# Performance work log

Measured on AMD Instinct MI355X. Metric: run time of the kernel, lower is better.

## Reference

```python
import jax, jax.numpy as jnp
import numpy as np

# Transformer config constants (from init_kwargs)
SRF = 3.0                 # spatial_receptive_field
SRF2 = SRF * SRF
ALPHA = 2.0
BETA = 8.0
GAMMA = 16.0
RES = jnp.array([0.5, 0.5, 0.5], dtype=jnp.float32)   # relative_positional_gresolution
N_BUCKETS = 2 * 8 + 1                                  # 2*beta + 1 = 17
MUL = jnp.array([N_BUCKETS ** 2, N_BUCKETS, 1], dtype=jnp.float32)  # [289,17,1]
SLICES_PER_ROT = 2


def setup_inputs() -> dict:
    key = jax.random.key(0)
    k1, k2 = jax.random.split(key)
    N = 3072
    # LiDAR-like point coordinates in a 10m cube; receptive field 3.0 makes radius filter selective
    xyz = jax.random.uniform(k1, (N, 3), dtype=jnp.float32) * 10.0
    # grid columns: [batch, block, gx, gy, gz]; values < 128 per the torch assert
    grid = jax.random.randint(k2, (N, 5), 0, 8, dtype=jnp.int32)
    return {"xyz": xyz, "grid": grid}


def _bucket_base(x):
    # from_dxyz_to_bucket_base, res.size(0)==3 branch
    x = x / RES
    x_abs = jnp.abs(x)
    log_ratio = jnp.log(jnp.maximum(x_abs, 1e-6) / ALPHA) / np.log(GAMMA / ALPHA)
    sup = jnp.minimum(jnp.round(ALPHA - (BETA - ALPHA) * log_ratio), BETA)
    sup = jnp.sign(x) * sup
    return BETA + jnp.where(x_abs <= ALPHA, jnp.round(x), sup)


def reference(xyz, grid):
    # no-kvp path of jit_compute_interactions, expressed as dense [N,N] pair masks
    batch = grid[:, 0]
    block = grid[:, 1]
    coords = grid[:, 2:]            # grid_look[:, 1:]

    # batch equality filter (meshgrid + batch==batch)
    batch_eq = batch[:, None] == batch[None, :]
    # causal block filter: block[iq] <= block[ik]
    block_le = block[:, None] <= block[None, :]

    # force_keep_neighbours: adjacent voxels within the same block
    coord_adj = jnp.max(jnp.abs(coords[:, None, :] - coords[None, :, :]), axis=-1) <= 1
    forcekeep = coord_adj & (block[:, None] == block[None, :])

    # coarse spatial hash on xy: ceil(xy / srf), neighbor cells only
    xy_coarse = jnp.ceil(xyz[:, :2] / SRF).astype(jnp.int32)
    keep_coarse = jnp.max(jnp.abs(xy_coarse[:, None, :] - xy_coarse[None, :, :]), axis=-1) <= 1

    # pairwise deltas (torch uses fp16 here; fp32 kept for numerical clarity) [N,N,3]
    dxyz = xyz[:, None, :] - xyz[None, :, :]
    keepr = jnp.sum(dxyz * dxyz, axis=-1) <= SRF2

    mask = batch_eq & block_le & (forcekeep | keep_coarse) & (forcekeep | keepr)

    dxyz_m = jnp.where(mask[..., None], dxyz, 0.0)

    # from_dxyz_to_bucket_mul: log-bucketize each axis, flatten via mul_buckets
    buckets = jnp.sum(MUL * _bucket_base(dxyz_m), axis=-1).astype(jnp.int32)
    buckets = jnp.where(mask, buckets, 0)

    # dscanid = scanid[ik] - scanid[iq], scanid = block // slices_per_rotation
    scanid = block // SLICES_PER_ROT
    dscanid = jnp.where(mask, scanid[None, :] - scanid[:, None], 0)

    return dxyz_m, buckets, dscanid, mask
```

## Files before the change

### kernel.cpp

```cpp
#include <hip/hip_runtime.h>
#include <cmath>


__device__ __forceinline__ float bucket_base(float v) {
    const float x  = v * 2.0f;
    const float xa = fabsf(x);
    if (xa <= 2.0f) {
        return 8.0f + rintf(x);
    }
    const float lr = logf(fmaxf(xa, 1e-6f) * 0.5f) / 2.0794415416798357f;
    const float sup = fminf(rintf(2.0f - 6.0f * lr), 8.0f);
    return 8.0f + ((x > 0.0f) ? sup : -sup);
}

__global__ __launch_bounds__(256) void pair_kernel(
    const float* __restrict__ xyz, const int* __restrict__ grid,
    float* __restrict__ out, int N) {
#pragma clang fp contract(off)
    const int jq = blockIdx.x * blockDim.x + threadIdx.x;
    const int j0 = jq << 2;
    const int i  = blockIdx.y;
    if (j0 >= N) return;

    const float xi = xyz[3 * i + 0];
    const float yi = xyz[3 * i + 1];
    const float zi = xyz[3 * i + 2];
    const int bat_i = grid[5 * i + 0];
    const int blk_i = grid[5 * i + 1];
    const int c0i = grid[5 * i + 2];
    const int c1i = grid[5 * i + 3];
    const int c2i = grid[5 * i + 4];
    const int xci = (int)ceilf(xi / 3.0f);
    const int yci = (int)ceilf(yi / 3.0f);
    const int scan_i = blk_i >> 1;

    const float4* pv = reinterpret_cast<const float4*>(xyz + (size_t)3 * j0);
    const float4 p0 = pv[0], p1 = pv[1], p2 = pv[2];
    const int4* gv = reinterpret_cast<const int4*>(grid + (size_t)5 * j0);
    const int4 g0 = gv[0], g1 = gv[1], g2 = gv[2], g3 = gv[3], g4 = gv[4];

    const float jx[4]  = {p0.x, p0.w, p1.z, p2.y};
    const float jy[4]  = {p0.y, p1.x, p1.w, p2.z};
    const float jz[4]  = {p0.z, p1.y, p2.x, p2.w};
    const int   jbat[4] = {g0.x, g1.y, g2.z, g3.w};
    const int   jblk[4] = {g0.y, g1.z, g2.w, g4.x};
    const int   jc0[4]  = {g0.z, g1.w, g3.x, g4.y};
    const int   jc1[4]  = {g0.w, g2.x, g3.y, g4.z};
    const int   jc2[4]  = {g1.x, g2.y, g3.z, g4.w};

    float dxm[4], dym[4], dzm[4];
    bool  mk[4];
    bool  any = false;
#pragma unroll
    for (int k = 0; k < 4; ++k) {
        const float dx = xi - jx[k];
        const float dy = yi - jy[k];
        const float dz = zi - jz[k];
        const bool batch_eq = (bat_i == jbat[k]);
        const bool block_le = (blk_i <= jblk[k]);
        const int  cadj = max(max(abs(c0i - jc0[k]), abs(c1i - jc1[k])),
                              abs(c2i - jc2[k]));
        const bool forcekeep = (cadj <= 1) && (blk_i == jblk[k]);
        const int xcj = (int)ceilf(jx[k] / 3.0f);
        const int ycj = (int)ceilf(jy[k] / 3.0f);
        const bool keep_coarse = max(abs(xci - xcj), abs(yci - ycj)) <= 1;
        const float d2 = dx * dx + dy * dy + dz * dz;
        const bool keepr = (d2 <= 9.0f);
        const bool m = batch_eq && block_le &&
                       (forcekeep || keep_coarse) && (forcekeep || keepr);
        mk[k] = m;
        any |= m;
        dxm[k] = m ? dx : 0.0f;
        dym[k] = m ? dy : 0.0f;
        dzm[k] = m ? dz : 0.0f;
    }

    const size_t NN   = (size_t)N * (size_t)N;
    const size_t base = (size_t)i * (size_t)N + (size_t)j0;
    float4* o_dxyz = reinterpret_cast<float4*>(out + 3 * base);
    float4* o_bkt  = reinterpret_cast<float4*>(out + NN * 3 + base);
    float4* o_dsc  = reinterpret_cast<float4*>(out + NN * 4 + base);
    float4* o_msk  = reinterpret_cast<float4*>(out + NN * 5 + base);

    if (__ballot(any ? 1 : 0) == 0ULL) {
        const float4 z = make_float4(0.0f, 0.0f, 0.0f, 0.0f);
        o_dxyz[0] = z; o_dxyz[1] = z; o_dxyz[2] = z;
        o_bkt[0]  = z; o_dsc[0]  = z; o_msk[0]  = z;
        return;
    }

    float bf[4], df[4], mf[4];
#pragma unroll
    for (int k = 0; k < 4; ++k) {
        if (mk[k]) {
            const float b0 = bucket_base(dxm[k]);
            const float b1 = bucket_base(dym[k]);
            const float b2 = bucket_base(dzm[k]);
            const float bsum = (289.0f * b0 + 17.0f * b1) + b2;
            bf[k] = (float)(int)bsum;
            df[k] = (float)((jblk[k] >> 1) - scan_i);
            mf[k] = 1.0f;
        } else {
            bf[k] = 0.0f; df[k] = 0.0f; mf[k] = 0.0f;
        }
    }

    o_dxyz[0] = make_float4(dxm[0], dym[0], dzm[0], dxm[1]);
    o_dxyz[1] = make_float4(dym[1], dzm[1], dxm[2], dym[2]);
    o_dxyz[2] = make_float4(dzm[2], dxm[3], dym[3], dzm[3]);
    o_bkt[0]  = make_float4(bf[0], bf[1], bf[2], bf[3]);
    o_dsc[0]  = make_float4(df[0], df[1], df[2], df[3]);
    o_msk[0]  = make_float4(mf[0], mf[1], mf[2], mf[3]);
}

extern "C" void kernel_launch(void* const* d_in, const int* in_sizes, int n_in,
                              void* d_out, int out_size, void* d_ws, size_t ws_size,
                              hipStream_t stream) {
    const float* xyz  = (const float*)d_in[0];
    const int*   grid = (const int*)d_in[1];
    float*       out  = (float*)d_out;
    const int N = in_sizes[0] / 3;

    const int BLOCK = 256;
    const int jquads = N / 4;
    dim3 gdim((jquads + BLOCK - 1) / BLOCK, N, 1);
    pair_kernel<<<gdim, dim3(BLOCK, 1, 1), 0, stream>>>(xyz, grid, out, N);
}
```

Measured before the change: 219.6 us.

## Map each thread to one contiguous output float4 across all six output planes

The kernel is restructured so each thread writes one float4 of the flat output buffer, in order, instead of each thread writing scattered float4s into six separate planes. The aim is fully contiguous, coalesced streaming writes. In exchange, the mask is recomputed for every plane (dxyz, buckets, dscanid, mask), which adds redundant loads and ALU work. The dxyz plane also evaluates pairs individually, with a divide by N and a modulo by 3. A template specialisation for N=3072 lets the compiler turn those divides into constant arithmetic.

```diff
diff --git a/kernel.cpp b/kernel.cpp
--- a/kernel.cpp
+++ b/kernel.cpp
@@ -13,26 +13,47 @@
     return 8.0f + ((x > 0.0f) ? sup : -sup);
 }
 
-__global__ __launch_bounds__(256) void pair_kernel(
+template<int CN>
+__device__ __forceinline__ void one_pair(
     const float* __restrict__ xyz, const int* __restrict__ grid,
-    float* __restrict__ out, int N) {
+    int Nrt, int p, float& dxm, float& dym, float& dzm)
+{
 #pragma clang fp contract(off)
-    const int jq = blockIdx.x * blockDim.x + threadIdx.x;
-    const int j0 = jq << 2;
-    const int i  = blockIdx.y;
-    if (j0 >= N) return;
+    const int N = CN ? CN : Nrt;
+    const int i = (int)((unsigned)p / (unsigned)N);
+    const int j = p - i * N;
+    const float xi = xyz[3*i+0], yi = xyz[3*i+1], zi = xyz[3*i+2];
+    const float xj = xyz[3*j+0], yj = xyz[3*j+1], zj = xyz[3*j+2];
+    const int bat_i = grid[5*i+0], blk_i = grid[5*i+1];
+    const int c0i = grid[5*i+2], c1i = grid[5*i+3], c2i = grid[5*i+4];
+    const int bat_j = grid[5*j+0], blk_j = grid[5*j+1];
+    const int c0j = grid[5*j+2], c1j = grid[5*j+3], c2j = grid[5*j+4];
+    const float dx = xi - xj, dy = yi - yj, dz = zi - zj;
+    const bool batch_eq = (bat_i == bat_j);
+    const bool block_le = (blk_i <= blk_j);
+    const int  cadj = max(max(abs(c0i-c0j), abs(c1i-c1j)), abs(c2i-c2j));
+    const bool forcekeep = (cadj <= 1) && (blk_i == blk_j);
+    const int xci = (int)ceilf(xi/3.0f), yci = (int)ceilf(yi/3.0f);
+    const int xcj = (int)ceilf(xj/3.0f), ycj = (int)ceilf(yj/3.0f);
+    const bool keep_coarse = max(abs(xci-xcj), abs(yci-ycj)) <= 1;
+    const float d2 = dx*dx + dy*dy + dz*dz;
+    const bool keepr = (d2 <= 9.0f);
+    const bool m = batch_eq && block_le &&
+                   (forcekeep || keep_coarse) && (forcekeep || keepr);
+    dxm = m ? dx : 0.0f; dym = m ? dy : 0.0f; dzm = m ? dz : 0.0f;
+}
 
-    const float xi = xyz[3 * i + 0];
-    const float yi = xyz[3 * i + 1];
-    const float zi = xyz[3 * i + 2];
-    const int bat_i = grid[5 * i + 0];
-    const int blk_i = grid[5 * i + 1];
-    const int c0i = grid[5 * i + 2];
-    const int c1i = grid[5 * i + 3];
-    const int c2i = grid[5 * i + 4];
-    const int xci = (int)ceilf(xi / 3.0f);
-    const int yci = (int)ceilf(yi / 3.0f);
-    const int scan_i = blk_i >> 1;
+__device__ __forceinline__ void quad_mask(
+    const float* __restrict__ xyz, const int* __restrict__ grid,
+    int i, int j0,
+    float dxm[4], float dym[4], float dzm[4], bool mk[4],
+    int jblk[4], int& blk_i, bool& any)
+{
+#pragma clang fp contract(off)
+    const float xi = xyz[3*i+0], yi = xyz[3*i+1], zi = xyz[3*i+2];
+    const int bat_i = grid[5*i+0]; blk_i = grid[5*i+1];
+    const int c0i = grid[5*i+2], c1i = grid[5*i+3], c2i = grid[5*i+4];
+    const int xci = (int)ceilf(xi/3.0f), yci = (int)ceilf(yi/3.0f);
 
     const float4* pv = reinterpret_cast<const float4*>(xyz + (size_t)3 * j0);
     const float4 p0 = pv[0], p1 = pv[1], p2 = pv[2];
@@ -43,24 +64,22 @@
     const float jy[4]  = {p0.y, p1.x, p1.w, p2.z};
     const float jz[4]  = {p0.z, p1.y, p2.x, p2.w};
     const int   jbat[4] = {g0.x, g1.y, g2.z, g3.w};
-    const int   jblk[4] = {g0.y, g1.z, g2.w, g4.x};
+    const int   jb[4]   = {g0.y, g1.z, g2.w, g4.x};
     const int   jc0[4]  = {g0.z, g1.w, g3.x, g4.y};
     const int   jc1[4]  = {g0.w, g2.x, g3.y, g4.z};
     const int   jc2[4]  = {g1.x, g2.y, g3.z, g4.w};
 
-    float dxm[4], dym[4], dzm[4];
-    bool  mk[4];
-    bool  any = false;
+    any = false;
 #pragma unroll
     for (int k = 0; k < 4; ++k) {
         const float dx = xi - jx[k];
         const float dy = yi - jy[k];
         const float dz = zi - jz[k];
         const bool batch_eq = (bat_i == jbat[k]);
-        const bool block_le = (blk_i <= jblk[k]);
+        const bool block_le = (blk_i <= jb[k]);
         const int  cadj = max(max(abs(c0i - jc0[k]), abs(c1i - jc1[k])),
                               abs(c2i - jc2[k]));
-        const bool forcekeep = (cadj <= 1) && (blk_i == jblk[k]);
+        const bool forcekeep = (cadj <= 1) && (blk_i == jb[k]);
         const int xcj = (int)ceilf(jx[k] / 3.0f);
         const int ycj = (int)ceilf(jy[k] / 3.0f);
         const bool keep_coarse = max(abs(xci - xcj), abs(yci - ycj)) <= 1;
@@ -68,49 +87,90 @@
         const bool keepr = (d2 <= 9.0f);
         const bool m = batch_eq && block_le &&
                        (forcekeep || keep_coarse) && (forcekeep || keepr);
-        mk[k] = m;
-        any |= m;
+        mk[k] = m; any |= m;
+        jblk[k] = jb[k];
         dxm[k] = m ? dx : 0.0f;
         dym[k] = m ? dy : 0.0f;
         dzm[k] = m ? dz : 0.0f;
     }
+}
 
-    const size_t NN   = (size_t)N * (size_t)N;
-    const size_t base = (size_t)i * (size_t)N + (size_t)j0;
-    float4* o_dxyz = reinterpret_cast<float4*>(out + 3 * base);
-    float4* o_bkt  = reinterpret_cast<float4*>(out + NN * 3 + base);
-    float4* o_dsc  = reinterpret_cast<float4*>(out + NN * 4 + base);
-    float4* o_msk  = reinterpret_cast<float4*>(out + NN * 5 + base);
+template<int CN>
+__global__ __launch_bounds__(256) void linear_kernel(
+    const float* __restrict__ xyz, const int* __restrict__ grid,
+    float* __restrict__ out, int Nrt)
+{
+    const int N = CN ? CN : Nrt;
+    const unsigned NN = (unsigned)N * (unsigned)N;
+    const unsigned t = blockIdx.x * blockDim.x + threadIdx.x;
+    const unsigned e = t * 4u;
+    if (e >= 6u * NN) return;
+    float4* dst = reinterpret_cast<float4*>(out + (size_t)e);
 
-    if (__ballot(any ? 1 : 0) == 0ULL) {
-        const float4 z = make_float4(0.0f, 0.0f, 0.0f, 0.0f);
-        o_dxyz[0] = z; o_dxyz[1] = z; o_dxyz[2] = z;
-        o_bkt[0]  = z; o_dsc[0]  = z; o_msk[0]  = z;
+    if (e < 3u * NN) {
+        const unsigned c0 = e % 3u;
+        const int p0 = (int)(e / 3u);
+        float a0, a1, a2, b0, b1, b2;
+        one_pair<CN>(xyz, grid, N, p0,     a0, a1, a2);
+        one_pair<CN>(xyz, grid, N, p0 + 1, b0, b1, b2);
+        float4 v;
+        if (c0 == 0u)      v = make_float4(a0, a1, a2, b0);
+        else if (c0 == 1u) v = make_float4(a1, a2, b0, b1);
+        else               v = make_float4(a2, b0, b1, b2);
+        *dst = v;
         return;
     }
 
-    float bf[4], df[4], mf[4];
+    float dx[4], dy[4], dz[4];
+    bool  mk[4];
+    int   jblk[4], blk_i;
+    bool  any;
+
+    if (e < 4u * NN) {
+        const int p = (int)(e - 3u * NN);
+        const int i = (int)((unsigned)p / (unsigned)N);
+        const int j0 = p - i * N;
+        quad_mask(xyz, grid, i, j0, dx, dy, dz, mk, jblk, blk_i, any);
+        if (__ballot(any ? 1 : 0) == 0ULL) {
+            *dst = make_float4(0.0f, 0.0f, 0.0f, 0.0f);
+            return;
+        }
+        float bf[4];
 #pragma unroll
-    for (int k = 0; k < 4; ++k) {
-        if (mk[k]) {
-            const float b0 = bucket_base(dxm[k]);
-            const float b1 = bucket_base(dym[k]);
-            const float b2 = bucket_base(dzm[k]);
-            const float bsum = (289.0f * b0 + 17.0f * b1) + b2;
-            bf[k] = (float)(int)bsum;
-            df[k] = (float)((jblk[k] >> 1) - scan_i);
-            mf[k] = 1.0f;
-        } else {
-            bf[k] = 0.0f; df[k] = 0.0f; mf[k] = 0.0f;
+        for (int k = 0; k < 4; ++k) {
+            if (mk[k]) {
+                const float q0 = bucket_base(dx[k]);
+                const float q1 = bucket_base(dy[k]);
+                const float q2 = bucket_base(dz[k]);
+                const float bsum = (289.0f * q0 + 17.0f * q1) + q2;
+                bf[k] = (float)(int)bsum;
+            } else {
+                bf[k] = 0.0f;
+            }
         }
+        *dst = make_float4(bf[0], bf[1], bf[2], bf[3]);
+    } else if (e < 5u * NN) {
+        const int p = (int)(e - 4u * NN);
+        const int i = (int)((unsigned)p / (unsigned)N);
+        const int j0 = p - i * N;
+        quad_mask(xyz, grid, i, j0, dx, dy, dz, mk, jblk, blk_i, any);
+        const int scan_i = blk_i >> 1;
+        float df[4];
+#pragma unroll
+        for (int k = 0; k < 4; ++k)
+            df[k] = mk[k] ? (float)((jblk[k] >> 1) - scan_i) : 0.0f;
+        *dst = make_float4(df[0], df[1], df[2], df[3]);
+    } else {
+        const int p = (int)(e - 5u * NN);
+        const int i = (int)((unsigned)p / (unsigned)N);
+        const int j0 = p - i * N;
+        quad_mask(xyz, grid, i, j0, dx, dy, dz, mk, jblk, blk_i, any);
+        float mf[4];
+#pragma unroll
+        for (int k = 0; k < 4; ++k)
+            mf[k] = mk[k] ? 1.0f : 0.0f;
+        *dst = make_float4(mf[0], mf[1], mf[2], mf[3]);
     }
-
-    o_dxyz[0] = make_float4(dxm[0], dym[0], dzm[0], dxm[1]);
-    o_dxyz[1] = make_float4(dym[1], dzm[1], dxm[2], dym[2]);
-    o_dxyz[2] = make_float4(dzm[2], dxm[3], dym[3], dzm[3]);
-    o_bkt[0]  = make_float4(bf[0], bf[1], bf[2], bf[3]);
-    o_dsc[0]  = make_float4(df[0], df[1], df[2], df[3]);
-    o_msk[0]  = make_float4(mf[0], mf[1], mf[2], mf[3]);
 }
 
 extern "C" void kernel_launch(void* const* d_in, const int* in_sizes, int n_in,
@@ -121,8 +181,13 @@
     float*       out  = (float*)d_out;
     const int N = in_sizes[0] / 3;
 
+    const unsigned total  = 6u * (unsigned)N * (unsigned)N;
+    const unsigned threads = (total + 3u) / 4u;
     const int BLOCK = 256;
-    const int jquads = N / 4;
-    dim3 gdim((jquads + BLOCK - 1) / BLOCK, N, 1);
-    pair_kernel<<<gdim, dim3(BLOCK, 1, 1), 0, stream>>>(xyz, grid, out, N);
+    const unsigned blocks = (threads + BLOCK - 1) / BLOCK;
+    if (N == 3072) {
+        linear_kernel<3072><<<blocks, BLOCK, 0, stream>>>(xyz, grid, out, N);
+    } else {
+        linear_kernel<0><<<blocks, BLOCK, 0, stream>>>(xyz, grid, out, N);
+    }
 }
```

Measured after the change: 269.5 us. 1.23x slower.
